# Optimization experiments

Hardware: AMD Instinct MI355X
Metric: run time of the kernel (lower is better)

## Reference

```python
import jax, jax.numpy as jnp
import numpy as np

N_NODES = 100000
D = 256
B = 1024
FANOUTS = [25, 10]  # sampling_size[0], sampling_size[1]


def _l2_normalize(h):
    # faithful to: h = h / norm if norm != 0 else h
    norm = jnp.linalg.norm(h, ord=2, axis=-1, keepdims=True)
    return h / jnp.where(norm == 0, 1.0, norm)


def setup_inputs() -> dict:
    key = jax.random.key(0)
    ks = jax.random.split(key, 8)
    features = jax.random.normal(ks[0], (N_NODES, D), dtype=jnp.float32)
    W0 = jax.random.normal(ks[1], (D, 2 * D), dtype=jnp.float32) * 0.05
    b0 = jax.random.normal(ks[2], (D,), dtype=jnp.float32) * 0.05
    W1 = jax.random.normal(ks[3], (D, 2 * D), dtype=jnp.float32) * 0.05
    b1 = jax.random.normal(ks[4], (D,), dtype=jnp.float32) * 0.05
    nodes2 = jax.random.randint(ks[5], (B,), 0, N_NODES, dtype=jnp.int32)
    neigh2 = jax.random.randint(ks[6], (B, FANOUTS[1]), 0, N_NODES, dtype=jnp.int32)
    n1 = B * (1 + FANOUTS[1])  # 11264
    neigh1 = jax.random.randint(ks[7], (n1, FANOUTS[0]), 0, N_NODES, dtype=jnp.int32)
    return {"features": features, "W0": W0, "b0": b0, "W1": W1, "b1": b1,
            "nodes2": nodes2, "neigh2": neigh2, "neigh1": neigh1}


def reference(features, W0, b0, W1, b1, nodes2, neigh2, neigh1):
    # Build node trees: nodes[k-1] = concat(nodes[k], neighbors(nodes[k]))
    nodes1 = jnp.concatenate([nodes2, neigh2.reshape(-1)])          # [n1]
    nodes0 = jnp.concatenate([nodes1, neigh1.reshape(-1)])          # [n0]
    n2, n1 = nodes2.shape[0], nodes1.shape[0]
    S0, S1 = neigh1.shape[1], neigh2.shape[1]

    h0 = features[nodes0]                                           # [n0, D] big gather

    # layer k=0: aggregate fan-out S0 neighbors (mean), concat self, linear, relu, l2
    self0 = h0[:n1]                                                 # [n1, D]
    agg0 = h0[n1:].reshape(n1, S0, -1).mean(axis=1)                 # [n1, D]
    h1 = jax.nn.relu(jnp.concatenate([self0, agg0], axis=-1) @ W0.T + b0)
    h1 = _l2_normalize(h1)                                          # [n1, D]

    # layer k=1
    self1 = h1[:n2]
    agg1 = h1[n2:].reshape(n2, S1, -1).mean(axis=1)
    h2 = jax.nn.relu(jnp.concatenate([self1, agg1], axis=-1) @ W1.T + b1)
    h2 = _l2_normalize(h2)                                          # [B, D]
    return h2
```

## Files before the change

### kernel.cpp

```cpp
#include <hip/hip_runtime.h>
#include <math.h>

#define D 256
#define K2 512
#define BATCH 1024
#define N1 11264
#define S0 25
#define S1 10

typedef __bf16 bf16x8 __attribute__((ext_vector_type(8)));
typedef __bf16 bf16x4 __attribute__((ext_vector_type(4)));
typedef float  f32x4  __attribute__((ext_vector_type(4)));

__global__ __launch_bounds__(256, 3) void fused_layer0(
        const float* __restrict__ feat, const float* __restrict__ W0,
        const float* __restrict__ b0, const int* __restrict__ nodes2,
        const int* __restrict__ neigh2, const int* __restrict__ neigh1,
        __bf16* __restrict__ h1b) {
    __shared__ __bf16 Atile[32 * 512];
    __shared__ __bf16 Bs[256 * 32];
    __shared__ float ssLDS[4][32];
    __shared__ float invLDS[32];

    const int tid = threadIdx.x;
    const int lane = tid & 63;
    const int w = tid >> 6;
    const int rl = lane & 15;
    const int g = lane >> 4;
    const int row0 = blockIdx.x * 32;

    float4 rb0[4], rb1[4];
#pragma unroll
    for (int s = 0; s < 4; ++s) {
        int i = tid + s * 256;
        int cg = i >> 6, kc = (i >> 4) & 3, lo = i & 15;
        const float* p = W0 + (size_t)(cg * 16 + lo) * K2 + kc * 8;
        rb0[s] = *(const float4*)p;
        rb1[s] = *(const float4*)(p + 4);
    }

#pragma unroll 1
    for (int r = w * 8; r < w * 8 + 8; ++r) {
        const int gr = row0 + r;
        const int self_idx = (gr < BATCH) ? nodes2[gr] : neigh2[gr - BATCH];
        const int* nb = neigh1 + (size_t)gr * S0;
        int idx[S0];
#pragma unroll
        for (int j = 0; j < S0; ++j) idx[j] = nb[j];
        float4 sv = ((const float4*)(feat + (size_t)self_idx * D))[lane];
        float4 v[S0];
#pragma unroll
        for (int j = 0; j < S0; ++j)
            v[j] = ((const float4*)(feat + (size_t)idx[j] * D))[lane];
        __builtin_amdgcn_sched_barrier(0);
        float4 acc = make_float4(0.f, 0.f, 0.f, 0.f);
#pragma unroll
        for (int j = 0; j < S0; ++j) {
            acc.x += v[j].x; acc.y += v[j].y; acc.z += v[j].z; acc.w += v[j].w;
        }
        const float s25 = 1.0f / 25.0f;
        bf16x4 svb = { (__bf16)sv.x, (__bf16)sv.y, (__bf16)sv.z, (__bf16)sv.w };
        bf16x4 avb = { (__bf16)(acc.x * s25), (__bf16)(acc.y * s25),
                       (__bf16)(acc.z * s25), (__bf16)(acc.w * s25) };
        const int sw = r & 7;
        const int gs = (lane >> 1) ^ sw;
        const int ga = (32 + (lane >> 1)) ^ sw;
        *(bf16x4*)(Atile + (size_t)r * 512 + gs * 8 + (lane & 1) * 4) = svb;
        *(bf16x4*)(Atile + (size_t)r * 512 + ga * 8 + (lane & 1) * 4) = avb;
    }
    __syncthreads();

    f32x4 acc[2][4];
#pragma unroll
    for (int rf = 0; rf < 2; ++rf)
#pragma unroll
        for (int nf = 0; nf < 4; ++nf) acc[rf][nf] = (f32x4){0.f, 0.f, 0.f, 0.f};

    for (int k0 = 0; k0 < K2; k0 += 32) {
#pragma unroll
        for (int s = 0; s < 4; ++s) {
            int i = tid + s * 256;
            bf16x8 bv;
            bv[0] = (__bf16)rb0[s].x; bv[1] = (__bf16)rb0[s].y;
            bv[2] = (__bf16)rb0[s].z; bv[3] = (__bf16)rb0[s].w;
            bv[4] = (__bf16)rb1[s].x; bv[5] = (__bf16)rb1[s].y;
            bv[6] = (__bf16)rb1[s].z; bv[7] = (__bf16)rb1[s].w;
            *(bf16x8*)(Bs + (size_t)i * 8) = bv;
        }
        __syncthreads();
        if (k0 + 32 < K2) {
#pragma unroll
            for (int s = 0; s < 4; ++s) {
                int i = tid + s * 256;
                int cg = i >> 6, kc = (i >> 4) & 3, lo = i & 15;
                const float* p = W0 + (size_t)(cg * 16 + lo) * K2 + (k0 + 32) + kc * 8;
                rb0[s] = *(const float4*)p;
                rb1[s] = *(const float4*)(p + 4);
            }
        }
        {
            const int gA = (k0 >> 3) + g;
            bf16x8 af[2], bfr[4];
#pragma unroll
            for (int rf = 0; rf < 2; ++rf) {
                int row = rf * 16 + rl;
                af[rf] = *(const bf16x8*)(Atile + (size_t)row * 512 +
                                          (size_t)(gA ^ (row & 7)) * 8);
            }
#pragma unroll
            for (int nf = 0; nf < 4; ++nf)
                bfr[nf] = *(const bf16x8*)(Bs + ((size_t)((w * 4 + nf) * 4 + g) * 16 + rl) * 8);
#pragma unroll
            for (int rf = 0; rf < 2; ++rf)
#pragma unroll
                for (int nf = 0; nf < 4; ++nf)
                    acc[rf][nf] = __builtin_amdgcn_mfma_f32_16x16x32_bf16(
                        af[rf], bfr[nf], acc[rf][nf], 0, 0, 0);
        }
        __syncthreads();
    }

    float bv[4];
#pragma unroll
    for (int nf = 0; nf < 4; ++nf) bv[nf] = b0[w * 64 + nf * 16 + rl];

#pragma unroll
    for (int rf = 0; rf < 2; ++rf) {
        float ss0 = 0.f, ss1 = 0.f, ss2 = 0.f, ss3 = 0.f;
#pragma unroll
        for (int nf = 0; nf < 4; ++nf) {
            float v0 = fmaxf(acc[rf][nf][0] + bv[nf], 0.f);
            float v1 = fmaxf(acc[rf][nf][1] + bv[nf], 0.f);
            float v2 = fmaxf(acc[rf][nf][2] + bv[nf], 0.f);
            float v3 = fmaxf(acc[rf][nf][3] + bv[nf], 0.f);
            acc[rf][nf][0] = v0; acc[rf][nf][1] = v1;
            acc[rf][nf][2] = v2; acc[rf][nf][3] = v3;
            ss0 += v0 * v0; ss1 += v1 * v1; ss2 += v2 * v2; ss3 += v3 * v3;
        }
#pragma unroll
        for (int m = 1; m < 16; m <<= 1) {
            ss0 += __shfl_xor(ss0, m);
            ss1 += __shfl_xor(ss1, m);
            ss2 += __shfl_xor(ss2, m);
            ss3 += __shfl_xor(ss3, m);
        }
        float ssv = (rl == 0) ? ss0 : (rl == 1) ? ss1 : (rl == 2) ? ss2 : ss3;
        if (rl < 4) ssLDS[w][rf * 16 + g * 4 + rl] = ssv;
    }
    __syncthreads();
    if (tid < 32) {
        float t = ssLDS[0][tid] + ssLDS[1][tid] + ssLDS[2][tid] + ssLDS[3][tid];
        invLDS[tid] = (t > 0.f) ? rsqrtf(t) : 1.0f;
    }
    __syncthreads();
#pragma unroll
    for (int rf = 0; rf < 2; ++rf)
#pragma unroll
        for (int j = 0; j < 4; ++j) {
            const int row = rf * 16 + g * 4 + j;
            const float inv = invLDS[row];
#pragma unroll
            for (int nf = 0; nf < 4; ++nf)
                h1b[(size_t)(row0 + row) * D + w * 64 + nf * 16 + rl] =
                    (__bf16)(acc[rf][nf][j] * inv);
        }
}

__global__ __launch_bounds__(256, 2) void fused_layer1(
        const __bf16* __restrict__ h1, const float* __restrict__ W1,
        const float* __restrict__ b1, float* __restrict__ Out) {
    constexpr int RB = 32;
    __shared__ __bf16 As[RB * 64];
    __shared__ __bf16 Bs[256 * 64];
    __shared__ float ssLDS[4][RB];
    __shared__ float invLDS[RB];

    const int tid = threadIdx.x;
    const int row0 = blockIdx.x * RB;
    const int lane = tid & 63;
    const int w = tid >> 6;
    const int rl = lane & 15;
    const int g = lane >> 4;
    const int rg = tid >> 7, kc8 = (tid >> 4) & 7, lo = tid & 15;
    const int grow = row0 + rg * 16 + lo;

    float4 rb0[8], rb1[8];
#pragma unroll
    for (int s = 0; s < 8; ++s) {
        int i = tid + s * 256;
        int cg = i >> 7, kc = (i >> 4) & 7, blo = i & 15;
        const float* p = W1 + (size_t)(cg * 16 + blo) * K2 + kc * 8;
        rb0[s] = *(const float4*)p;
        rb1[s] = *(const float4*)(p + 4);
    }

    f32x4 acc[2][4];
#pragma unroll
    for (int rf = 0; rf < 2; ++rf)
#pragma unroll
        for (int nf = 0; nf < 4; ++nf) acc[rf][nf] = (f32x4){0.f, 0.f, 0.f, 0.f};

    for (int k0 = 0; k0 < K2; k0 += 64) {
        bf16x8 av;
        if (k0 < 256) {
            av = *(const bf16x8*)(h1 + (size_t)grow * D + k0 + kc8 * 8);
        } else {
            float f[8];
#pragma unroll
            for (int e = 0; e < 8; ++e) f[e] = 0.f;
            const __bf16* base = h1 + (size_t)(BATCH + grow * S1) * D + (k0 - 256) + kc8 * 8;
#pragma unroll
            for (int j = 0; j < S1; ++j) {
                bf16x8 vv = *(const bf16x8*)(base + (size_t)j * D);
#pragma unroll
                for (int e = 0; e < 8; ++e) f[e] += (float)vv[e];
            }
#pragma unroll
            for (int e = 0; e < 8; ++e) av[e] = (__bf16)(f[e] * 0.1f);
        }
        *(bf16x8*)(As + (size_t)tid * 8) = av;
#pragma unroll
        for (int s = 0; s < 8; ++s) {
            int i = tid + s * 256;
            bf16x8 bb;
            bb[0] = (__bf16)rb0[s].x; bb[1] = (__bf16)rb0[s].y;
            bb[2] = (__bf16)rb0[s].z; bb[3] = (__bf16)rb0[s].w;
            bb[4] = (__bf16)rb1[s].x; bb[5] = (__bf16)rb1[s].y;
            bb[6] = (__bf16)rb1[s].z; bb[7] = (__bf16)rb1[s].w;
            *(bf16x8*)(Bs + (size_t)i * 8) = bb;
        }
        __syncthreads();
        if (k0 + 64 < K2) {
#pragma unroll
            for (int s = 0; s < 8; ++s) {
                int i = tid + s * 256;
                int cg = i >> 7, kc = (i >> 4) & 7, blo = i & 15;
                const float* p = W1 + (size_t)(cg * 16 + blo) * K2 + (k0 + 64) + kc * 8;
                rb0[s] = *(const float4*)p;
                rb1[s] = *(const float4*)(p + 4);
            }
        }
#pragma unroll
        for (int kf = 0; kf < 2; ++kf) {
            const int kc = kf * 4 + g;
            bf16x8 af[2], bfr[4];
#pragma unroll
            for (int rf = 0; rf < 2; ++rf)
                af[rf] = *(const bf16x8*)(As + ((size_t)(rf * 8 + kc) * 16 + rl) * 8);
#pragma unroll
            for (int nf = 0; nf < 4; ++nf)
                bfr[nf] = *(const bf16x8*)(Bs + ((size_t)((w * 4 + nf) * 8 + kc) * 16 + rl) * 8);
#pragma unroll
            for (int rf = 0; rf < 2; ++rf)
#pragma unroll
                for (int nf = 0; nf < 4; ++nf)
                    acc[rf][nf] = __builtin_amdgcn_mfma_f32_16x16x32_bf16(
                        af[rf], bfr[nf], acc[rf][nf], 0, 0, 0);
        }
        __syncthreads();
    }

    float bv[4];
#pragma unroll
    for (int nf = 0; nf < 4; ++nf) bv[nf] = b1[w * 64 + nf * 16 + rl];

#pragma unroll
    for (int rf = 0; rf < 2; ++rf) {
        float ss0 = 0.f, ss1 = 0.f, ss2 = 0.f, ss3 = 0.f;
#pragma unroll
        for (int nf = 0; nf < 4; ++nf) {
            float v0 = fmaxf(acc[rf][nf][0] + bv[nf], 0.f);
            float v1 = fmaxf(acc[rf][nf][1] + bv[nf], 0.f);
            float v2 = fmaxf(acc[rf][nf][2] + bv[nf], 0.f);
            float v3 = fmaxf(acc[rf][nf][3] + bv[nf], 0.f);
            acc[rf][nf][0] = v0; acc[rf][nf][1] = v1;
            acc[rf][nf][2] = v2; acc[rf][nf][3] = v3;
            ss0 += v0 * v0; ss1 += v1 * v1; ss2 += v2 * v2; ss3 += v3 * v3;
        }
#pragma unroll
        for (int m = 1; m < 16; m <<= 1) {
            ss0 += __shfl_xor(ss0, m);
            ss1 += __shfl_xor(ss1, m);
            ss2 += __shfl_xor(ss2, m);
            ss3 += __shfl_xor(ss3, m);
        }
        float ssv = (rl == 0) ? ss0 : (rl == 1) ? ss1 : (rl == 2) ? ss2 : ss3;
        if (rl < 4) ssLDS[w][rf * 16 + g * 4 + rl] = ssv;
    }
    __syncthreads();
    if (tid < RB) {
        float t = ssLDS[0][tid] + ssLDS[1][tid] + ssLDS[2][tid] + ssLDS[3][tid];
        invLDS[tid] = (t > 0.f) ? rsqrtf(t) : 1.0f;
    }
    __syncthreads();
#pragma unroll
    for (int rf = 0; rf < 2; ++rf)
#pragma unroll
        for (int j = 0; j < 4; ++j) {
            const int row = rf * 16 + g * 4 + j;
            const float inv = invLDS[row];
#pragma unroll
            for (int nf = 0; nf < 4; ++nf)
                Out[(size_t)(row0 + row) * D + w * 64 + nf * 16 + rl] = acc[rf][nf][j] * inv;
        }
}

extern "C" void kernel_launch(void* const* d_in, const int* in_sizes, int n_in,
                              void* d_out, int out_size, void* d_ws, size_t ws_size,
                              hipStream_t stream) {
    const float* features = (const float*)d_in[0];
    const float* W0       = (const float*)d_in[1];
    const float* b0       = (const float*)d_in[2];
    const float* W1       = (const float*)d_in[3];
    const float* b1       = (const float*)d_in[4];
    const int*   nodes2   = (const int*)d_in[5];
    const int*   neigh2   = (const int*)d_in[6];
    const int*   neigh1   = (const int*)d_in[7];
    float* out = (float*)d_out;

    __bf16* h1b = (__bf16*)d_ws;

    fused_layer0<<<N1 / 32, 256, 0, stream>>>(features, W0, b0, nodes2, neigh2,
                                              neigh1, h1b);
    fused_layer1<<<BATCH / 32, 256, 0, stream>>>(h1b, W1, b1, out);
}
```

Baseline: 102.5 us.

## Split layer0 into gather-producer and GEMM-consumer warps with double-buffered weights

Layer-0 blocks grow to 512 threads. Four warps gather and mean the neighbor features into the LDS A tile, while four consumer warps stage the first W0 tile and then spin on an LDS counter until all rows are ready. The W0 tile in LDS is now double-buffered, and consumer-only sync uses atomic counters instead of __syncthreads. This is meant to overlap the W0 load with the gather and cut barrier cost in the GEMM loop. In exchange it adds spin-wait overhead, more threads per block, and limits on occupancy. The GEMM still cannot start until the whole gather finishes.

```diff
diff --git a/kernel.cpp b/kernel.cpp
--- a/kernel.cpp
+++ b/kernel.cpp
@@ -12,15 +12,18 @@
 typedef __bf16 bf16x4 __attribute__((ext_vector_type(4)));
 typedef float  f32x4  __attribute__((ext_vector_type(4)));
 
-__global__ __launch_bounds__(256, 3) void fused_layer0(
+#define WG __HIP_MEMORY_SCOPE_WORKGROUP
+
+__global__ __launch_bounds__(512, 4) void fused_layer0_pc(
         const float* __restrict__ feat, const float* __restrict__ W0,
         const float* __restrict__ b0, const int* __restrict__ nodes2,
         const int* __restrict__ neigh2, const int* __restrict__ neigh1,
         __bf16* __restrict__ h1b) {
     __shared__ __bf16 Atile[32 * 512];
-    __shared__ __bf16 Bs[256 * 32];
+    __shared__ __bf16 Bs[2][256 * 32];
     __shared__ float ssLDS[4][32];
-    __shared__ float invLDS[32];
+    __shared__ int rowcnt;
+    __shared__ int rbar;
 
     const int tid = threadIdx.x;
     const int lane = tid & 63;
@@ -29,69 +32,99 @@
     const int g = lane >> 4;
     const int row0 = blockIdx.x * 32;
 
+    if (tid == 0) { rowcnt = 0; rbar = 0; }
+    __syncthreads();
+
+    if (w < 4) {
+#pragma unroll 1
+        for (int r = w * 8; r < w * 8 + 8; ++r) {
+            const int gr = row0 + r;
+            const int self_idx = (gr < BATCH) ? nodes2[gr] : neigh2[gr - BATCH];
+            const int* nb = neigh1 + (size_t)gr * S0;
+            int idx[S0];
+#pragma unroll
+            for (int j = 0; j < S0; ++j) idx[j] = nb[j];
+            float4 sv = ((const float4*)(feat + (size_t)self_idx * D))[lane];
+            float4 v[S0];
+#pragma unroll
+            for (int j = 0; j < S0; ++j)
+                v[j] = ((const float4*)(feat + (size_t)idx[j] * D))[lane];
+            __builtin_amdgcn_sched_barrier(0);
+            float4 acc = make_float4(0.f, 0.f, 0.f, 0.f);
+#pragma unroll
+            for (int j = 0; j < S0; ++j) {
+                acc.x += v[j].x; acc.y += v[j].y; acc.z += v[j].z; acc.w += v[j].w;
+            }
+            const float s25 = 1.0f / 25.0f;
+            bf16x4 svb = { (__bf16)sv.x, (__bf16)sv.y, (__bf16)sv.z, (__bf16)sv.w };
+            bf16x4 avb = { (__bf16)(acc.x * s25), (__bf16)(acc.y * s25),
+                           (__bf16)(acc.z * s25), (__bf16)(acc.w * s25) };
+            const int sw = r & 7;
+            const int gs = (lane >> 1) ^ sw;
+            const int ga = (32 + (lane >> 1)) ^ sw;
+            *(bf16x4*)(Atile + (size_t)r * 512 + gs * 8 + (lane & 1) * 4) = svb;
+            *(bf16x4*)(Atile + (size_t)r * 512 + ga * 8 + (lane & 1) * 4) = avb;
+            asm volatile("s_waitcnt lgkmcnt(0)" ::: "memory");
+            if (lane == 0)
+                __hip_atomic_fetch_add(&rowcnt, 1, __ATOMIC_RELEASE, WG);
+        }
+        return;
+    }
+
+    const int cw = w - 4;
+    const int ctid = tid - 256;
+
     float4 rb0[4], rb1[4];
 #pragma unroll
     for (int s = 0; s < 4; ++s) {
-        int i = tid + s * 256;
+        int i = ctid + s * 256;
         int cg = i >> 6, kc = (i >> 4) & 3, lo = i & 15;
         const float* p = W0 + (size_t)(cg * 16 + lo) * K2 + kc * 8;
         rb0[s] = *(const float4*)p;
         rb1[s] = *(const float4*)(p + 4);
     }
+#pragma unroll
+    for (int s = 0; s < 4; ++s) {
+        int i = ctid + s * 256;
+        bf16x8 bv;
+        bv[0] = (__bf16)rb0[s].x; bv[1] = (__bf16)rb0[s].y;
+        bv[2] = (__bf16)rb0[s].z; bv[3] = (__bf16)rb0[s].w;
+        bv[4] = (__bf16)rb1[s].x; bv[5] = (__bf16)rb1[s].y;
+        bv[6] = (__bf16)rb1[s].z; bv[7] = (__bf16)rb1[s].w;
+        *(bf16x8*)(&Bs[0][0] + (size_t)i * 8) = bv;
+    }
+
+    while (__hip_atomic_load(&rowcnt, __ATOMIC_ACQUIRE, WG) < 32)
+        __builtin_amdgcn_s_sleep(2);
+    __builtin_amdgcn_sched_barrier(0);
+
+    int round = 0;
+#define CSYNC()                                                            \
+    do {                                                                   \
+        ++round;                                                           \
+        asm volatile("s_waitcnt lgkmcnt(0)" ::: "memory");                 \
+        if (lane == 0)                                                     \
+            __hip_atomic_fetch_add(&rbar, 1, __ATOMIC_RELEASE, WG);        \
+        while (__hip_atomic_load(&rbar, __ATOMIC_ACQUIRE, WG) < 4 * round) \
+            __builtin_amdgcn_s_sleep(1);                                   \
+        __builtin_amdgcn_sched_barrier(0);                                 \
+    } while (0)
+
+    CSYNC();
+
+    f32x4 acc[2][4];
+#pragma unroll
+    for (int rf = 0; rf < 2; ++rf)
+#pragma unroll
+        for (int nf = 0; nf < 4; ++nf) acc[rf][nf] = (f32x4){0.f, 0.f, 0.f, 0.f};
 
 #pragma unroll 1
-    for (int r = w * 8; r < w * 8 + 8; ++r) {
-        const int gr = row0 + r;
-        const int self_idx = (gr < BATCH) ? nodes2[gr] : neigh2[gr - BATCH];
-        const int* nb = neigh1 + (size_t)gr * S0;
-        int idx[S0];
-#pragma unroll
-        for (int j = 0; j < S0; ++j) idx[j] = nb[j];
-        float4 sv = ((const float4*)(feat + (size_t)self_idx * D))[lane];
-        float4 v[S0];
-#pragma unroll
-        for (int j = 0; j < S0; ++j)
-            v[j] = ((const float4*)(feat + (size_t)idx[j] * D))[lane];
-        __builtin_amdgcn_sched_barrier(0);
-        float4 acc = make_float4(0.f, 0.f, 0.f, 0.f);
-#pragma unroll
-        for (int j = 0; j < S0; ++j) {
-            acc.x += v[j].x; acc.y += v[j].y; acc.z += v[j].z; acc.w += v[j].w;
-        }
-        const float s25 = 1.0f / 25.0f;
-        bf16x4 svb = { (__bf16)sv.x, (__bf16)sv.y, (__bf16)sv.z, (__bf16)sv.w };
-        bf16x4 avb = { (__bf16)(acc.x * s25), (__bf16)(acc.y * s25),
-                       (__bf16)(acc.z * s25), (__bf16)(acc.w * s25) };
-        const int sw = r & 7;
-        const int gs = (lane >> 1) ^ sw;
-        const int ga = (32 + (lane >> 1)) ^ sw;
-        *(bf16x4*)(Atile + (size_t)r * 512 + gs * 8 + (lane & 1) * 4) = svb;
-        *(bf16x4*)(Atile + (size_t)r * 512 + ga * 8 + (lane & 1) * 4) = avb;
-    }
-    __syncthreads();
-
-    f32x4 acc[2][4];
-#pragma unroll
-    for (int rf = 0; rf < 2; ++rf)
-#pragma unroll
-        for (int nf = 0; nf < 4; ++nf) acc[rf][nf] = (f32x4){0.f, 0.f, 0.f, 0.f};
-
-    for (int k0 = 0; k0 < K2; k0 += 32) {
-#pragma unroll
-        for (int s = 0; s < 4; ++s) {
-            int i = tid + s * 256;
-            bf16x8 bv;
-            bv[0] = (__bf16)rb0[s].x; bv[1] = (__bf16)rb0[s].y;
-            bv[2] = (__bf16)rb0[s].z; bv[3] = (__bf16)rb0[s].w;
-            bv[4] = (__bf16)rb1[s].x; bv[5] = (__bf16)rb1[s].y;
-            bv[6] = (__bf16)rb1[s].z; bv[7] = (__bf16)rb1[s].w;
-            *(bf16x8*)(Bs + (size_t)i * 8) = bv;
-        }
-        __syncthreads();
-        if (k0 + 32 < K2) {
+    for (int t = 0; t < 16; ++t) {
+        const int k0 = t * 32;
+        if (t < 15) {
 #pragma unroll
             for (int s = 0; s < 4; ++s) {
-                int i = tid + s * 256;
+                int i = ctid + s * 256;
                 int cg = i >> 6, kc = (i >> 4) & 3, lo = i & 15;
                 const float* p = W0 + (size_t)(cg * 16 + lo) * K2 + (k0 + 32) + kc * 8;
                 rb0[s] = *(const float4*)p;
@@ -109,7 +142,8 @@
             }
 #pragma unroll
             for (int nf = 0; nf < 4; ++nf)
-                bfr[nf] = *(const bf16x8*)(Bs + ((size_t)((w * 4 + nf) * 4 + g) * 16 + rl) * 8);
+                bfr[nf] = *(const bf16x8*)(&Bs[t & 1][0] +
+                           ((size_t)((cw * 4 + nf) * 4 + g) * 16 + rl) * 8);
 #pragma unroll
             for (int rf = 0; rf < 2; ++rf)
 #pragma unroll
@@ -117,12 +151,24 @@
                     acc[rf][nf] = __builtin_amdgcn_mfma_f32_16x16x32_bf16(
                         af[rf], bfr[nf], acc[rf][nf], 0, 0, 0);
         }
-        __syncthreads();
+        if (t < 15) {
+#pragma unroll
+            for (int s = 0; s < 4; ++s) {
+                int i = ctid + s * 256;
+                bf16x8 bv;
+                bv[0] = (__bf16)rb0[s].x; bv[1] = (__bf16)rb0[s].y;
+                bv[2] = (__bf16)rb0[s].z; bv[3] = (__bf16)rb0[s].w;
+                bv[4] = (__bf16)rb1[s].x; bv[5] = (__bf16)rb1[s].y;
+                bv[6] = (__bf16)rb1[s].z; bv[7] = (__bf16)rb1[s].w;
+                *(bf16x8*)(&Bs[(t + 1) & 1][0] + (size_t)i * 8) = bv;
+            }
+        }
+        CSYNC();
     }
 
     float bv[4];
 #pragma unroll
-    for (int nf = 0; nf < 4; ++nf) bv[nf] = b0[w * 64 + nf * 16 + rl];
+    for (int nf = 0; nf < 4; ++nf) bv[nf] = b0[cw * 64 + nf * 16 + rl];
 
 #pragma unroll
     for (int rf = 0; rf < 2; ++rf) {
@@ -145,25 +191,22 @@
             ss3 += __shfl_xor(ss3, m);
         }
         float ssv = (rl == 0) ? ss0 : (rl == 1) ? ss1 : (rl == 2) ? ss2 : ss3;
-        if (rl < 4) ssLDS[w][rf * 16 + g * 4 + rl] = ssv;
-    }
-    __syncthreads();
-    if (tid < 32) {
-        float t = ssLDS[0][tid] + ssLDS[1][tid] + ssLDS[2][tid] + ssLDS[3][tid];
-        invLDS[tid] = (t > 0.f) ? rsqrtf(t) : 1.0f;
-    }
-    __syncthreads();
+        if (rl < 4) ssLDS[cw][rf * 16 + g * 4 + rl] = ssv;
+    }
+    CSYNC();
 #pragma unroll
     for (int rf = 0; rf < 2; ++rf)
 #pragma unroll
         for (int j = 0; j < 4; ++j) {
             const int row = rf * 16 + g * 4 + j;
-            const float inv = invLDS[row];
+            float t = ssLDS[0][row] + ssLDS[1][row] + ssLDS[2][row] + ssLDS[3][row];
+            const float inv = (t > 0.f) ? rsqrtf(t) : 1.0f;
 #pragma unroll
             for (int nf = 0; nf < 4; ++nf)
-                h1b[(size_t)(row0 + row) * D + w * 64 + nf * 16 + rl] =
+                h1b[(size_t)(row0 + row) * D + cw * 64 + nf * 16 + rl] =
                     (__bf16)(acc[rf][nf][j] * inv);
         }
+#undef CSYNC
 }
 
 __global__ __launch_bounds__(256, 2) void fused_layer1(
@@ -320,7 +363,7 @@
 
     __bf16* h1b = (__bf16*)d_ws;
 
-    fused_layer0<<<N1 / 32, 256, 0, stream>>>(features, W0, b0, nodes2, neigh2,
-                                              neigh1, h1b);
+    fused_layer0_pc<<<N1 / 32, 512, 0, stream>>>(features, W0, b0, nodes2,
+                                                 neigh2, neigh1, h1b);
     fused_layer1<<<BATCH / 32, 256, 0, stream>>>(h1b, W1, b1, out);
 }
```

New measurement: 102.7 us. No clear change (+0.2%).
